# Optimization experiments

Measured on AMD Instinct MI355X. Metric: run time of the kernel, lower is better.

The kernel has to match this reference:

```python
import jax, jax.numpy as jnp
import numpy as np

B, N, D = 32, 181, 512          # batch, num_projs (seq len), embed_dim
H, HD = 8, 64                   # heads, head_dim
DEPTH, FFN = 6, 2048            # layers, mlp_ratio*embed_dim
MAXLEN = 181                    # RPE max_len (EncoderLayer default)
LN_EPS = 1e-5


def setup_inputs() -> dict:
    key = jax.random.key(0)
    ks = jax.random.split(key, 16)
    rn = lambda k, s, sc=0.02: (jax.random.normal(k, s, jnp.float32) * sc)
    return {
        "x_0": jax.random.normal(ks[0], (B, N, D), jnp.float32),
        "max_shift": 50,
        "pos_embed": rn(ks[1], (1, N, D)),
        "qkv_w": rn(ks[2], (DEPTH, D, 3 * D)), "qkv_b": jnp.zeros((DEPTH, 3 * D), jnp.float32),
        "out_w": rn(ks[3], (DEPTH, D, D)), "out_b": jnp.zeros((DEPTH, D), jnp.float32),
        "rel_pos": jax.random.normal(ks[4], (DEPTH, 2 * MAXLEN - 1, HD), jnp.float32),
        "rpe_w": rn(ks[5], (DEPTH, HD, 1)),
        "ln1_g": jnp.ones((DEPTH, D), jnp.float32), "ln1_b": jnp.zeros((DEPTH, D), jnp.float32),
        "ffn_w1": rn(ks[6], (DEPTH, D, FFN)), "ffn_b1": jnp.zeros((DEPTH, FFN), jnp.float32),
        "ffn_w2": rn(ks[7], (DEPTH, FFN, D)), "ffn_b2": jnp.zeros((DEPTH, D), jnp.float32),
        "ln2_g": jnp.ones((DEPTH, D), jnp.float32), "ln2_b": jnp.zeros((DEPTH, D), jnp.float32),
        "mlp_w1": rn(ks[8], (D, 64)), "mlp_b1": jnp.zeros((64,), jnp.float32),
        "mlp_w2": rn(ks[9], (64, 1)), "mlp_b2": jnp.zeros((1,), jnp.float32),
    }


def _layer_norm(x, g, b):
    m = jnp.mean(x, -1, keepdims=True)
    v = jnp.mean((x - m) ** 2, -1, keepdims=True)
    return (x - m) * jax.lax.rsqrt(v + LN_EPS) * g + b


def reference(x_0, max_shift, pos_embed, qkv_w, qkv_b, out_w, out_b, rel_pos, rpe_w,
              ln1_g, ln1_b, ffn_w1, ffn_b1, ffn_w2, ffn_b2, ln2_g, ln2_b,
              mlp_w1, mlp_b1, mlp_w2, mlp_b2):
    Bb, T, L = x_0.shape
    n_head = H
    hd = L // n_head
    scale = hd ** -0.5
    max_len = (rel_pos.shape[1] + 1) // 2
    # relative position index table [T, T]
    idx = jnp.arange(T)[None, :] - jnp.arange(T)[:, None] + (max_len - 1)

    x = x_0 + pos_embed
    depth = qkv_w.shape[0]
    for i in range(depth):
        # --- MHA with relative position bias ---
        qkv = (x @ qkv_w[i] + qkv_b[i]).reshape(Bb, T, 3, n_head, hd)
        q, k, v = qkv[:, :, 0], qkv[:, :, 1], qkv[:, :, 2]   # [B,T,H,hd]
        scores = jnp.einsum('bqhd,bkhd->bhqk', q, k) * scale
        bias = (rel_pos[i][idx] @ rpe_w[i])[..., 0]          # [T,T]
        scores = scores + bias[None, None]
        w = jax.nn.softmax(scores, axis=-1)
        attn = jnp.einsum('bhqk,bkhd->bqhd', w, v).reshape(Bb, T, L)
        attn = attn @ out_w[i] + out_b[i]
        x = _layer_norm(x + attn, ln1_g[i], ln1_b[i])
        # --- FFN ---
        h = jax.nn.gelu(x @ ffn_w1[i] + ffn_b1[i], approximate=False)
        h = h @ ffn_w2[i] + ffn_b2[i]
        x = _layer_norm(x + h, ln2_g[i], ln2_b[i])

    # per-projection shift head
    shift = jax.nn.relu(x @ mlp_w1 + mlp_b1) @ mlp_w2 + mlp_b2   # [B,T,1]

    # --- SpatialTransformer: bilinear warp along L only (flow[:,0] == 0) ---
    grid_y = 2.0 * (jnp.arange(T, dtype=jnp.float32) / (T - 1) - 0.5)   # [T]
    grid_x = 2.0 * (jnp.arange(L, dtype=jnp.float32) / (L - 1) - 0.5)   # [L]
    flow_x = shift * max_shift / (L // 2)                               # [B,T,1]
    gx = grid_x[None, None, :] + flow_x                                 # [B,T,L]
    # unnormalize (align_corners=False), border padding -> clamp coords
    ix = jnp.clip(((gx + 1.0) * L - 1.0) / 2.0, 0.0, L - 1.0)
    iy = jnp.clip(((grid_y + 1.0) * T - 1.0) / 2.0, 0.0, T - 1.0)       # [T]
    ix0f = jnp.floor(ix); wx = ix - ix0f
    iy0f = jnp.floor(iy); wy = iy - iy0f
    ix0 = jnp.clip(ix0f.astype(jnp.int32), 0, L - 1)
    ix1 = jnp.clip(ix0 + 1, 0, L - 1)
    iy0 = jnp.clip(iy0f.astype(jnp.int32), 0, T - 1)
    iy1 = jnp.clip(iy0 + 1, 0, T - 1)
    bidx = jnp.arange(Bb)[:, None, None]
    iy0b, iy1b = iy0[None, :, None], iy1[None, :, None]
    v00 = x_0[bidx, iy0b, ix0]; v01 = x_0[bidx, iy0b, ix1]
    v10 = x_0[bidx, iy1b, ix0]; v11 = x_0[bidx, iy1b, ix1]
    wyb = wy[None, :, None]
    warped = (1 - wyb) * ((1 - wx) * v00 + wx * v01) + wyb * ((1 - wx) * v10 + wx * v11)
    return shift, warped
```

## Files before the change

### kernel.cpp

```cpp
#include <hip/hip_runtime.h>
#include <hip/hip_bf16.h>
#include <math.h>

#define M_ROWS 5792
#define NTOK 181
#define NLAYER 6

typedef __attribute__((ext_vector_type(8))) _Float16 f16x8;
typedef __attribute__((ext_vector_type(4))) float f32x4;
typedef __attribute__((ext_vector_type(16))) float f32x16;

__device__ __forceinline__ ushort f2h(float f) {
    union { _Float16 h; ushort u; } v;
    v.h = (_Float16)f;
    return v.u;
}
__device__ __forceinline__ float h2f(ushort u) {
    union { ushort u; _Float16 h; } v; v.u = u;
    return (float)v.h;
}
__device__ __forceinline__ float gelu_f(float v) {
    return 0.5f * v * (1.0f + erff(v * 0.70710678118654752f));
}
__device__ __forceinline__ void async16(const void* g, void* l) {
    __builtin_amdgcn_global_load_lds((const __attribute__((address_space(1))) void*)g,
                                     (__attribute__((address_space(3))) void*)l, 16, 0, 0);
}

__global__ __launch_bounds__(256) void wt_kernel(const float* __restrict__ W,
                                                 ushort* __restrict__ Wt, int K, int N) {
    __shared__ float t[64][65];
    const size_t ls = (size_t)blockIdx.z * K * N;
    const float* Wl = W + ls;
    ushort* Wtl = Wt + ls;
    const int k0 = blockIdx.x * 64, n0 = blockIdx.y * 64;
    const int tr = threadIdx.x >> 6, tc = threadIdx.x & 63;
    #pragma unroll
    for (int i = 0; i < 16; ++i) {
        const int r = i * 4 + tr;
        t[r][tc] = Wl[(size_t)(k0 + r) * N + n0 + tc];
    }
    __syncthreads();
    #pragma unroll
    for (int i = 0; i < 16; ++i) {
        const int r = i * 4 + tr;
        Wtl[(size_t)(n0 + r) * K + k0 + tc] = f2h(t[tc][r]);
    }
}

__global__ void add_pos_kernel(const float* __restrict__ x0, const float* __restrict__ pos,
                               float* __restrict__ x, ushort* __restrict__ xb) {
    int idx = blockIdx.x * 256 + threadIdx.x;
    const int total = M_ROWS * 128;
    if (idx >= total) return;
    int col = idx & 127;
    int m   = idx >> 7;
    int t   = m % NTOK;
    float4 a = ((const float4*)x0)[idx];
    float4 p = ((const float4*)pos)[t * 128 + col];
    a.x += p.x; a.y += p.y; a.z += p.z; a.w += p.w;
    ((float4*)x)[idx] = a;
    ((ushort4*)xb)[idx] = make_ushort4(f2h(a.x), f2h(a.y), f2h(a.z), f2h(a.w));
}

template<int BM, int EPI, int SK>
__global__ __launch_bounds__(256) void mfma_gemm(const ushort* __restrict__ A,
                                                 const ushort* __restrict__ Bt,
                                                 const float* __restrict__ bias,
                                                 void* __restrict__ Cv,
                                                 int M, int K, int N) {
    constexpr int MREP = BM / 32;
    __shared__ __align__(16) ushort sA[2][BM * 32];
    __shared__ __align__(16) ushort sB[2][128 * 32];

    const int NC  = N >> 7;
    const int NR  = (M + BM - 1) / BM;
    const int NRP = (NR + 7) & ~7;
    const int PSB = NRP * NC;
    const int gid = blockIdx.x;
    const int sk  = (SK > 1) ? gid / PSB : 0;
    const int j   = (SK > 1) ? gid % PSB : gid;
    const int r   = (j / (8 * NC)) * 8 + (j & 7);
    const int c   = (j % (8 * NC)) >> 3;
    if (r >= NR) return;

    const int tid = threadIdx.x;
    const int lane = tid & 63;
    const int w = tid >> 6;
    const int wr = w >> 1, wc = w & 1;
    const int row0 = r * BM, col0 = c * 128;
    const int wbase = tid & ~63;

    f32x4 acc[MREP][4];
    const f32x4 zero = {0.f, 0.f, 0.f, 0.f};
    #pragma unroll
    for (int m = 0; m < MREP; ++m)
        #pragma unroll
        for (int n = 0; n < 4; ++n) acc[m][n] = zero;

    auto stage = [&](int buf, int kt) {
        const int k0 = kt << 5;
        #pragma unroll
        for (int i = 0; i < BM / 64; ++i) {
            const int s = i * 256 + tid;
            const int row = s >> 2;
            const int kbl = (s & 3) ^ ((row >> 1) & 3);
            int gr = row0 + row; if (gr > M - 1) gr = M - 1;
            async16(A + (size_t)gr * K + k0 + (kbl << 3),
                    &sA[buf][(i * 256 + wbase) * 8]);
        }
        #pragma unroll
        for (int i = 0; i < 2; ++i) {
            const int s = i * 256 + tid;
            const int nr = s >> 2;
            const int kbl = (s & 3) ^ ((nr >> 1) & 3);
            async16(Bt + (size_t)(col0 + nr) * K + k0 + (kbl << 3),
                    &sB[buf][(i * 256 + wbase) * 8]);
        }
    };

    const int NIT = (K / SK) >> 5;
    const int kt0 = sk * NIT;
    stage(0, kt0);
    const int l15 = lane & 15, kb = lane >> 4;
    for (int it = 0; it < NIT; ++it) {
        __syncthreads();
        if (it + 1 < NIT) stage((it + 1) & 1, kt0 + it + 1);
        const int buf = it & 1;
        f16x8 af[MREP], bfr[4];
        #pragma unroll
        for (int m = 0; m < MREP; ++m) {
            const int rr = wr * (BM / 2) + m * 16 + l15;
            af[m] = *(const f16x8*)&sA[buf][rr * 32 + ((kb ^ ((rr >> 1) & 3)) << 3)];
        }
        #pragma unroll
        for (int n = 0; n < 4; ++n) {
            const int rr = wc * 64 + n * 16 + l15;
            bfr[n] = *(const f16x8*)&sB[buf][rr * 32 + ((kb ^ ((rr >> 1) & 3)) << 3)];
        }
        #pragma unroll
        for (int m = 0; m < MREP; ++m)
            #pragma unroll
            for (int n = 0; n < 4; ++n)
                acc[m][n] = __builtin_amdgcn_mfma_f32_16x16x32_f16(af[m], bfr[n], acc[m][n], 0, 0, 0);
    }

    const int crow = row0 + wr * (BM / 2) + (lane >> 4) * 4;
    const int ccol = col0 + wc * 64 + l15;
    ushort* outh = (ushort*)Cv + (size_t)sk * M * N;
    #pragma unroll
    for (int m = 0; m < MREP; ++m)
        #pragma unroll
        for (int n = 0; n < 4; ++n) {
            const int gc = ccol + n * 16;
            const float bv = (SK == 1 || sk == 0) ? bias[gc] : 0.f;
            #pragma unroll
            for (int rr = 0; rr < 4; ++rr) {
                const int gr = crow + m * 16 + rr;
                if (gr < M) {
                    float v = acc[m][n][rr] + bv;
                    if (EPI == 1)      outh[(size_t)gr * N + gc] = f2h(gelu_f(v));
                    else if (EPI == 2) outh[(size_t)gr * N + gc] = f2h(v);
                    else               ((float*)Cv)[(size_t)gr * N + gc] = v;
                }
            }
        }
}

__global__ __launch_bounds__(256) void head_mfma(const ushort* __restrict__ A,
                                                 const ushort* __restrict__ Bt,
                                                 const float* __restrict__ b1,
                                                 const float* __restrict__ w2,
                                                 const float* __restrict__ b2,
                                                 float* __restrict__ shift) {
    const int M = M_ROWS, K = 512;
    __shared__ __align__(16) ushort sA[2][128 * 32];
    __shared__ __align__(16) ushort sB[2][64 * 32];
    const int tid = threadIdx.x;
    const int lane = tid & 63;
    const int w = tid >> 6;
    const int row0 = blockIdx.x * 128;
    const int wbase = tid & ~63;

    f32x4 acc[2][4];
    const f32x4 zero = {0.f, 0.f, 0.f, 0.f};
    #pragma unroll
    for (int m = 0; m < 2; ++m)
        #pragma unroll
        for (int n = 0; n < 4; ++n) acc[m][n] = zero;

    auto stage = [&](int buf, int kt) {
        const int k0 = kt << 5;
        #pragma unroll
        for (int i = 0; i < 2; ++i) {
            const int s = i * 256 + tid;
            const int row = s >> 2;
            const int kbl = (s & 3) ^ ((row >> 1) & 3);
            int gr = row0 + row; if (gr > M - 1) gr = M - 1;
            async16(A + (size_t)gr * K + k0 + (kbl << 3),
                    &sA[buf][(i * 256 + wbase) * 8]);
        }
        {
            const int s = tid;
            const int nr = s >> 2;
            const int kbl = (s & 3) ^ ((nr >> 1) & 3);
            async16(Bt + (size_t)nr * K + k0 + (kbl << 3),
                    &sB[buf][wbase * 8]);
        }
    };

    stage(0, 0);
    const int l15 = lane & 15, kb = lane >> 4;
    for (int it = 0; it < 16; ++it) {
        __syncthreads();
        if (it + 1 < 16) stage((it + 1) & 1, it + 1);
        const int buf = it & 1;
        f16x8 af[2], bfr[4];
        #pragma unroll
        for (int m = 0; m < 2; ++m) {
            const int r = w * 32 + m * 16 + l15;
            af[m] = *(const f16x8*)&sA[buf][r * 32 + ((kb ^ ((r >> 1) & 3)) << 3)];
        }
        #pragma unroll
        for (int n = 0; n < 4; ++n) {
            const int r = n * 16 + l15;
            bfr[n] = *(const f16x8*)&sB[buf][r * 32 + ((kb ^ ((r >> 1) & 3)) << 3)];
        }
        #pragma unroll
        for (int m = 0; m < 2; ++m)
            #pragma unroll
            for (int n = 0; n < 4; ++n)
                acc[m][n] = __builtin_amdgcn_mfma_f32_16x16x32_f16(af[m], bfr[n], acc[m][n], 0, 0, 0);
    }

    const float b2v = b2[0];
    float b1v[4], w2v[4];
    #pragma unroll
    for (int n = 0; n < 4; ++n) {
        const int c = n * 16 + l15;
        b1v[n] = b1[c];
        w2v[n] = w2[c];
    }
    #pragma unroll
    for (int m = 0; m < 2; ++m) {
        #pragma unroll
        for (int r = 0; r < 4; ++r) {
            float p = 0.f;
            #pragma unroll
            for (int n = 0; n < 4; ++n)
                p += fmaxf(acc[m][n][r] + b1v[n], 0.f) * w2v[n];
            #pragma unroll
            for (int off = 1; off < 16; off <<= 1) p += __shfl_xor(p, off);
            const int gr = row0 + w * 32 + m * 16 + kb * 4 + r;
            if (l15 == 0 && gr < M) shift[gr] = p + b2v;
        }
    }
}

__global__ void rbias_kernel(const float* __restrict__ rel_pos, const float* __restrict__ rpe_w,
                             float* __restrict__ r) {
    const int l = blockIdx.y;
    int j = blockIdx.x * 64 + threadIdx.x;
    if (j >= 2 * NTOK - 1) return;
    const float* rp = rel_pos + ((size_t)l * (2 * NTOK - 1) + j) * 64;
    const float* wv = rpe_w + l * 64;
    float s = 0.f;
    #pragma unroll
    for (int d = 0; d < 64; d += 4) {
        float4 a = *(const float4*)(rp + d);
        float4 b = *(const float4*)(wv + d);
        s += a.x*b.x + a.y*b.y + a.z*b.z + a.w*b.w;
    }
    r[l * 512 + j] = s;
}

__global__ __launch_bounds__(192, 2) void attn_mfma(const ushort* __restrict__ qkv,
                                                    const float* __restrict__ rb,
                                                    ushort* __restrict__ outb) {
    __shared__ __align__(16) ushort sm[18432];
    __shared__ __align__(16) ushort vt[12288];
    __shared__ float rs[416];
    const int b  = blockIdx.x >> 4;
    const int h  = (blockIdx.x >> 1) & 7;
    const int qh = blockIdx.x & 1;
    const int tid = threadIdx.x, lane = tid & 63, w = tid >> 6;
    const int l31 = lane & 31, hi = lane >> 5;
    const ushort* base = qkv + (size_t)(b * NTOK) * 1536 + h * 64;

    for (int i = tid; i < 416; i += 192) {
        int j = i - 32;
        rs[i] = (j >= 0 && j < 2 * NTOK - 1) ? rb[j] : 0.f;
    }
    #pragma unroll
    for (int i = 0; i < 8; ++i) {
        const int c = i * 192 + w * 64 + lane;
        const int k = c >> 3;
        int kg = k; if (kg > NTOK - 1) kg = NTOK - 1;
        const int dc = (c & 7) ^ (k & 7);
        async16(base + (size_t)kg * 1536 + 512 + dc * 8, &sm[(i * 192 + w * 64) * 8]);
    }
    #pragma unroll
    for (int i = 0; i < 4; ++i) {
        const int c = i * 192 + w * 64 + lane;
        const int ql = c >> 3;
        int qg = qh * 96 + ql; if (qg > NTOK - 1) qg = NTOK - 1;
        const int dc = (c & 7) ^ (ql & 7);
        async16(base + (size_t)qg * 1536 + dc * 8, &sm[12288 + (i * 192 + w * 64) * 8]);
    }
    #pragma unroll
    for (int i = 0; i < 8; ++i) {
        const int c = tid + i * 192;
        const int k = c >> 3, dcc = c & 7;
        const int kk = k < NTOK ? k : NTOK - 1;
        const uint4 v = *(const uint4*)(base + (size_t)kk * 1536 + 1024 + dcc * 8);
        const uint vv[4] = {v.x, v.y, v.z, v.w};
        #pragma unroll
        for (int j = 0; j < 4; ++j) {
            const int d0 = dcc * 8 + j * 2, d1 = d0 + 1;
            vt[d0 * 192 + ((((k >> 3) ^ ((d0 ^ (d0 >> 3)) & 7)) << 3) + (k & 7))] = (ushort)(vv[j] & 0xffffu);
            vt[d1 * 192 + ((((k >> 3) ^ ((d1 ^ (d1 >> 3)) & 7)) << 3) + (k & 7))] = (ushort)(vv[j] >> 16);
        }
    }
    __syncthreads();

    const int ql = 32 * w + l31;
    const int q  = qh * 96 + ql;
    f16x8 qf[4];
    #pragma unroll
    for (int ds = 0; ds < 4; ++ds)
        qf[ds] = *(const f16x8*)&sm[12288 + ql * 64 + (((2 * ds + hi) ^ (ql & 7)) << 3)];

    f32x16 S[6];
    #pragma unroll
    for (int kt = 0; kt < 6; ++kt)
        #pragma unroll
        for (int r = 0; r < 16; ++r) S[kt][r] = 0.f;
    #pragma unroll
    for (int kt = 0; kt < 6; ++kt) {
        const int krow = kt * 32 + l31;
        #pragma unroll
        for (int ds = 0; ds < 4; ++ds) {
            f16x8 kf = *(const f16x8*)&sm[krow * 64 + (((2 * ds + hi) ^ (krow & 7)) << 3)];
            S[kt] = __builtin_amdgcn_mfma_f32_32x32x16_f16(kf, qf[ds], S[kt], 0, 0, 0);
        }
    }

    float mx = -1e30f;
    #pragma unroll
    for (int kt = 0; kt < 6; ++kt)
        #pragma unroll
        for (int r = 0; r < 16; ++r) {
            const int k = kt * 32 + (r & 3) + 8 * (r >> 2) + 4 * hi;
            float s = (k < NTOK) ? S[kt][r] * 0.125f + rs[k - q + 212] : -1e30f;
            S[kt][r] = s;
            mx = fmaxf(mx, s);
        }
    mx = fmaxf(mx, __shfl_xor(mx, 32));
    float sum = 0.f;
    #pragma unroll
    for (int kt = 0; kt < 6; ++kt)
        #pragma unroll
        for (int r = 0; r < 16; ++r) {
            float e = __expf(S[kt][r] - mx);
            S[kt][r] = e;
            sum += e;
        }
    sum += __shfl_xor(sum, 32);
    const float inv = 1.0f / sum;

    __syncthreads();

    const int sq = (l31 ^ (l31 >> 3)) & 7;
    #pragma unroll
    for (int kt = 0; kt < 6; ++kt)
        #pragma unroll
        for (int r = 0; r < 16; r += 2) {
            const int k = kt * 32 + (r & 3) + 8 * (r >> 2) + 4 * hi;
            const uint pk = (uint)f2h(S[kt][r] * inv) | ((uint)f2h(S[kt][r + 1] * inv) << 16);
            *(uint*)&sm[w * 6144 + l31 * 192 + ((((k >> 3) ^ sq) << 3) + (k & 7))] = pk;
        }
    __syncthreads();

    f32x16 O[2];
    #pragma unroll
    for (int nt = 0; nt < 2; ++nt)
        #pragma unroll
        for (int r = 0; r < 16; ++r) O[nt][r] = 0.f;
    #pragma unroll
    for (int kt2 = 0; kt2 < 12; ++kt2) {
        f16x8 pa = *(const f16x8*)&sm[w * 6144 + l31 * 192 + ((((2 * kt2 + hi) ^ sq) << 3))];
        #pragma unroll
        for (int nt = 0; nt < 2; ++nt) {
            const int d = nt * 32 + l31;
            f16x8 vf = *(const f16x8*)&vt[d * 192 + (((2 * kt2 + hi) ^ ((d ^ (d >> 3)) & 7)) << 3)];
            O[nt] = __builtin_amdgcn_mfma_f32_32x32x16_f16(pa, vf, O[nt], 0, 0, 0);
        }
    }

    #pragma unroll
    for (int nt = 0; nt < 2; ++nt)
        #pragma unroll
        for (int r = 0; r < 16; ++r) {
            const int qr = qh * 96 + 32 * w + (r & 3) + 8 * (r >> 2) + 4 * hi;
            if (qr < NTOK)
                outb[(size_t)(b * NTOK + qr) * 512 + h * 64 + nt * 32 + l31] = f2h(O[nt][r]);
        }
}

template<int NY>
__global__ __launch_bounds__(256) void lnres_kernel(float* __restrict__ x, ushort* __restrict__ xb,
                                                    const ushort* __restrict__ y,
                                                    const ushort* __restrict__ y1,
                                                    const float* __restrict__ g, const float* __restrict__ bb) {
    const int row = blockIdx.x * 4 + (threadIdx.x >> 6);
    const int l = threadIdx.x & 63;
    float* xr = x + (size_t)row * 512;
    ushort* xbr = xb + (size_t)row * 512;
    const ushort* yr = y + (size_t)row * 512;
    float4 v0 = *(const float4*)(xr + (l << 2));
    float4 v1 = *(const float4*)(xr + 256 + (l << 2));
    const ushort4 u0 = *(const ushort4*)(yr + (l << 2));
    const ushort4 u1 = *(const ushort4*)(yr + 256 + (l << 2));
    v0.x += h2f(u0.x); v0.y += h2f(u0.y); v0.z += h2f(u0.z); v0.w += h2f(u0.w);
    v1.x += h2f(u1.x); v1.y += h2f(u1.y); v1.z += h2f(u1.z); v1.w += h2f(u1.w);
    if (NY == 2) {
        const ushort* y1r = y1 + (size_t)row * 512;
        const ushort4 w0 = *(const ushort4*)(y1r + (l << 2));
        const ushort4 w1 = *(const ushort4*)(y1r + 256 + (l << 2));
        v0.x += h2f(w0.x); v0.y += h2f(w0.y); v0.z += h2f(w0.z); v0.w += h2f(w0.w);
        v1.x += h2f(w1.x); v1.y += h2f(w1.y); v1.z += h2f(w1.z); v1.w += h2f(w1.w);
    }
    float s = v0.x + v0.y + v0.z + v0.w + v1.x + v1.y + v1.z + v1.w;
    #pragma unroll
    for (int off = 32; off; off >>= 1) s += __shfl_xor(s, off);
    const float m = s * (1.0f / 512.0f);
    float d0 = v0.x - m, d1 = v0.y - m, d2 = v0.z - m, d3 = v0.w - m;
    float d4 = v1.x - m, d5 = v1.y - m, d6 = v1.z - m, d7 = v1.w - m;
    float q = d0*d0 + d1*d1 + d2*d2 + d3*d3 + d4*d4 + d5*d5 + d6*d6 + d7*d7;
    #pragma unroll
    for (int off = 32; off; off >>= 1) q += __shfl_xor(q, off);
    const float r = rsqrtf(q * (1.0f / 512.0f) + 1e-5f);
    const float4 g0 = *(const float4*)(g + (l << 2));
    const float4 g1 = *(const float4*)(g + 256 + (l << 2));
    const float4 b0 = *(const float4*)(bb + (l << 2));
    const float4 b1 = *(const float4*)(bb + 256 + (l << 2));
    float4 o0, o1;
    o0.x = d0 * r * g0.x + b0.x; o0.y = d1 * r * g0.y + b0.y;
    o0.z = d2 * r * g0.z + b0.z; o0.w = d3 * r * g0.w + b0.w;
    o1.x = d4 * r * g1.x + b1.x; o1.y = d5 * r * g1.y + b1.y;
    o1.z = d6 * r * g1.z + b1.z; o1.w = d7 * r * g1.w + b1.w;
    *(float4*)(xr + (l << 2)) = o0;
    *(float4*)(xr + 256 + (l << 2)) = o1;
    *(ushort4*)(xbr + (l << 2)) = make_ushort4(f2h(o0.x), f2h(o0.y), f2h(o0.z), f2h(o0.w));
    *(ushort4*)(xbr + 256 + (l << 2)) = make_ushort4(f2h(o1.x), f2h(o1.y), f2h(o1.z), f2h(o1.w));
}

__global__ void warp_kernel(const float* __restrict__ x0, const float* __restrict__ shift,
                            const int* __restrict__ pms, float* __restrict__ warped) {
    int idx = blockIdx.x * 256 + threadIdx.x;
    if (idx >= M_ROWS * 512) return;
    int c = idx & 511;
    int m = idx >> 9;
    int t = m % NTOK;
    int b = m / NTOK;
    float max_shift = (float)pms[0];
    float sh = shift[m];
    float flow = sh * max_shift / 256.0f;
    float gx = 2.0f * ((float)c / 511.0f - 0.5f) + flow;
    float ix = ((gx + 1.0f) * 512.0f - 1.0f) * 0.5f;
    ix = fminf(fmaxf(ix, 0.0f), 511.0f);
    float gy = 2.0f * ((float)t / 180.0f - 0.5f);
    float iy = ((gy + 1.0f) * 181.0f - 1.0f) * 0.5f;
    iy = fminf(fmaxf(iy, 0.0f), 180.0f);
    float ix0f = floorf(ix), iy0f = floorf(iy);
    float wx = ix - ix0f, wy = iy - iy0f;
    int ix0 = min(max((int)ix0f, 0), 511);
    int ix1 = min(ix0 + 1, 511);
    int iy0 = min(max((int)iy0f, 0), 180);
    int iy1 = min(iy0 + 1, 180);
    const float* xb = x0 + (size_t)b * NTOK * 512;
    float v00 = xb[iy0 * 512 + ix0], v01 = xb[iy0 * 512 + ix1];
    float v10 = xb[iy1 * 512 + ix0], v11 = xb[iy1 * 512 + ix1];
    warped[idx] = (1.f - wy) * ((1.f - wx) * v00 + wx * v01) + wy * ((1.f - wx) * v10 + wx * v11);
}

extern "C" void kernel_launch(void* const* d_in, const int* in_sizes, int n_in,
                              void* d_out, int out_size, void* d_ws, size_t ws_size,
                              hipStream_t stream) {
    const float* x0   = (const float*)d_in[0];
    const int*   pms  = (const int*)d_in[1];
    const float* pos  = (const float*)d_in[2];
    const float* qkvw = (const float*)d_in[3];
    const float* qkvb = (const float*)d_in[4];
    const float* outw = (const float*)d_in[5];
    const float* outbp= (const float*)d_in[6];
    const float* relp = (const float*)d_in[7];
    const float* rpew = (const float*)d_in[8];
    const float* ln1g = (const float*)d_in[9];
    const float* ln1b = (const float*)d_in[10];
    const float* fw1  = (const float*)d_in[11];
    const float* fb1  = (const float*)d_in[12];
    const float* fw2  = (const float*)d_in[13];
    const float* fb2  = (const float*)d_in[14];
    const float* ln2g = (const float*)d_in[15];
    const float* ln2b = (const float*)d_in[16];
    const float* mw1  = (const float*)d_in[17];
    const float* mb1  = (const float*)d_in[18];
    const float* mw2  = (const float*)d_in[19];
    const float* mb2  = (const float*)d_in[20];

    float* out = (float*)d_out;

    char* ws = (char*)d_ws;
    float*  x     = (float*)ws;
    ushort* xb    = (ushort*)(ws + 11862016);
    char*   qr    = ws + 11862016 + 5931008;
    ushort* qkv   = (ushort*)qr;
    ushort* ybuf  = (ushort*)qr;
    ushort* ybuf2 = (ushort*)(qr + 5931008);
    ushort* hbuf  = (ushort*)(qr + 11862016);
    ushort* attnb = (ushort*)(qr + 35586048);
    float*  rbias = (float*)(qr + 35586048 + 5931008);
    ushort* wts   = (ushort*)(qr + 35586048 + 5931008 + 12288);
    ushort* qkv_wt = wts;
    ushort* out_wt = qkv_wt + 6 * 1536 * 512;
    ushort* f1_wt  = out_wt + 6 * 512 * 512;
    ushort* f2_wt  = f1_wt  + 6 * 512 * 2048;
    ushort* w1t    = f2_wt  + 6 * 2048 * 512;

    wt_kernel<<<dim3(8, 24, 6), 256, 0, stream>>>(qkvw, qkv_wt, 512, 1536);
    wt_kernel<<<dim3(8,  8, 6), 256, 0, stream>>>(outw, out_wt, 512, 512);
    wt_kernel<<<dim3(8, 32, 6), 256, 0, stream>>>(fw1,  f1_wt,  512, 2048);
    wt_kernel<<<dim3(32, 8, 6), 256, 0, stream>>>(fw2,  f2_wt,  2048, 512);
    wt_kernel<<<dim3(8,  1, 1), 256, 0, stream>>>(mw1,  w1t,    512, 64);
    rbias_kernel<<<dim3(6, 6), 64, 0, stream>>>(relp, rpew, rbias);

    add_pos_kernel<<<(M_ROWS * 128 + 255) / 256, 256, 0, stream>>>(x0, pos, x, xb);

    const int g_qkv  = 96 * 12;
    const int g_ffn1 = 96 * 16;
    const int g_np4  = 96 * 4;
    for (int i = 0; i < NLAYER; ++i) {
        mfma_gemm<64, 2, 1><<<g_qkv, 256, 0, stream>>>(xb, qkv_wt + (size_t)i * 1536 * 512,
                                                       qkvb + i * 1536, qkv, M_ROWS, 512, 1536);
        attn_mfma<<<512, 192, 0, stream>>>(qkv, rbias + i * 512, attnb);
        mfma_gemm<64, 2, 2><<<g_np4 * 2, 256, 0, stream>>>(attnb, out_wt + (size_t)i * 512 * 512,
                                                           outbp + i * 512, ybuf, M_ROWS, 512, 512);
        lnres_kernel<2><<<1448, 256, 0, stream>>>(x, xb, ybuf, ybuf2, ln1g + i * 512, ln1b + i * 512);
        mfma_gemm<64, 1, 1><<<g_ffn1, 256, 0, stream>>>(xb, f1_wt + (size_t)i * 2048 * 512,
                                                        fb1 + i * 2048, hbuf, M_ROWS, 512, 2048);
        mfma_gemm<64, 2, 2><<<g_np4 * 2, 256, 0, stream>>>(hbuf, f2_wt + (size_t)i * 512 * 2048,
                                                           fb2 + i * 512, ybuf, M_ROWS, 2048, 512);
        lnres_kernel<2><<<1448, 256, 0, stream>>>(x, xb, ybuf, ybuf2, ln2g + i * 512, ln2b + i * 512);
    }

    head_mfma<<<46, 256, 0, stream>>>(xb, w1t, mb1, mw2, mb2, out);
    warp_kernel<<<(M_ROWS * 512 + 255) / 256, 256, 0, stream>>>(x0, out, pms, out + M_ROWS);
}
```

Measured before the change: 786.8 us.

## Keep softmax probabilities in registers and vectorize V transpose into LDS

The attention kernel no longer writes P to LDS and reads it back. It builds the MFMA A-operand directly from the S accumulator registers with cross-half-wave shuffles, which removes two __syncthreads barriers. The V transpose now has each thread load 8 rows and write packed 16-byte chunks, replacing the scattered 2-byte LDS stores. s_setprio is also raised around the MFMA loops; the cost is more register pressure and extra shuffle instructions.

```diff
diff --git a/kernel.cpp b/kernel.cpp
--- a/kernel.cpp
+++ b/kernel.cpp
@@ -307,18 +307,29 @@
         const int dc = (c & 7) ^ (ql & 7);
         async16(base + (size_t)qg * 1536 + dc * 8, &sm[12288 + (i * 192 + w * 64) * 8]);
     }
-    #pragma unroll
-    for (int i = 0; i < 8; ++i) {
-        const int c = tid + i * 192;
-        const int k = c >> 3, dcc = c & 7;
-        const int kk = k < NTOK ? k : NTOK - 1;
-        const uint4 v = *(const uint4*)(base + (size_t)kk * 1536 + 1024 + dcc * 8);
-        const uint vv[4] = {v.x, v.y, v.z, v.w};
-        #pragma unroll
-        for (int j = 0; j < 4; ++j) {
-            const int d0 = dcc * 8 + j * 2, d1 = d0 + 1;
-            vt[d0 * 192 + ((((k >> 3) ^ ((d0 ^ (d0 >> 3)) & 7)) << 3) + (k & 7))] = (ushort)(vv[j] & 0xffffu);
-            vt[d1 * 192 + ((((k >> 3) ^ ((d1 ^ (d1 >> 3)) & 7)) << 3) + (k & 7))] = (ushort)(vv[j] >> 16);
+    {
+        const int k8 = tid % 24;
+        const int dc = tid / 24;
+        uint4 rowv[8];
+        #pragma unroll
+        for (int i = 0; i < 8; ++i) {
+            int kk = k8 * 8 + i; if (kk > NTOK - 1) kk = NTOK - 1;
+            rowv[i] = *(const uint4*)(base + (size_t)kk * 1536 + 1024 + dc * 8);
+        }
+        #pragma unroll
+        for (int j = 0; j < 8; ++j) {
+            const int d = dc * 8 + j;
+            const int sd = (d ^ (d >> 3)) & 7;
+            uint out[4];
+            #pragma unroll
+            for (int m = 0; m < 4; ++m) {
+                const uint lo  = ((const uint*)&rowv[2 * m    ])[j >> 1];
+                const uint hi2 = ((const uint*)&rowv[2 * m + 1])[j >> 1];
+                const uint a = (j & 1) ? (lo  >> 16) : (lo  & 0xffffu);
+                const uint bb = (j & 1) ? (hi2 >> 16) : (hi2 & 0xffffu);
+                out[m] = a | (bb << 16);
+            }
+            *(uint4*)&vt[d * 192 + ((k8 ^ sd) << 3)] = *(uint4*)out;
         }
     }
     __syncthreads();
@@ -335,6 +346,7 @@
     for (int kt = 0; kt < 6; ++kt)
         #pragma unroll
         for (int r = 0; r < 16; ++r) S[kt][r] = 0.f;
+    __builtin_amdgcn_s_setprio(1);
     #pragma unroll
     for (int kt = 0; kt < 6; ++kt) {
         const int krow = kt * 32 + l31;
@@ -344,6 +356,7 @@
             S[kt] = __builtin_amdgcn_mfma_f32_32x32x16_f16(kf, qf[ds], S[kt], 0, 0, 0);
         }
     }
+    __builtin_amdgcn_s_setprio(0);
 
     float mx = -1e30f;
     #pragma unroll
@@ -367,19 +380,10 @@
         }
     sum += __shfl_xor(sum, 32);
     const float inv = 1.0f / sum;
-
-    __syncthreads();
-
-    const int sq = (l31 ^ (l31 >> 3)) & 7;
     #pragma unroll
     for (int kt = 0; kt < 6; ++kt)
         #pragma unroll
-        for (int r = 0; r < 16; r += 2) {
-            const int k = kt * 32 + (r & 3) + 8 * (r >> 2) + 4 * hi;
-            const uint pk = (uint)f2h(S[kt][r] * inv) | ((uint)f2h(S[kt][r + 1] * inv) << 16);
-            *(uint*)&sm[w * 6144 + l31 * 192 + ((((k >> 3) ^ sq) << 3) + (k & 7))] = pk;
-        }
-    __syncthreads();
+        for (int r = 0; r < 16; ++r) S[kt][r] *= inv;
 
     f32x16 O[2];
     #pragma unroll
@@ -388,13 +392,28 @@
         for (int r = 0; r < 16; ++r) O[nt][r] = 0.f;
     #pragma unroll
     for (int kt2 = 0; kt2 < 12; ++kt2) {
-        f16x8 pa = *(const f16x8*)&sm[w * 6144 + l31 * 192 + ((((2 * kt2 + hi) ^ sq) << 3))];
+        const int kt = kt2 >> 1, half = kt2 & 1;
+        uint p[4];
+        #pragma unroll
+        for (int m = 0; m < 4; ++m)
+            p[m] = (uint)f2h(S[kt][8 * half + 2 * m]) |
+                   ((uint)f2h(S[kt][8 * half + 2 * m + 1]) << 16);
+        const uint s0l = (uint)__shfl_xor((int)p[0], 32);
+        const uint s0h = (uint)__shfl_xor((int)p[1], 32);
+        const uint s1l = (uint)__shfl_xor((int)p[2], 32);
+        const uint s1h = (uint)__shfl_xor((int)p[3], 32);
+        uint fa[4];
+        if (hi == 0) { fa[0] = p[0]; fa[1] = p[1]; fa[2] = s0l; fa[3] = s0h; }
+        else         { fa[0] = s1l; fa[1] = s1h; fa[2] = p[2]; fa[3] = p[3]; }
+        const f16x8 pa = *(const f16x8*)fa;
+        __builtin_amdgcn_s_setprio(1);
         #pragma unroll
         for (int nt = 0; nt < 2; ++nt) {
             const int d = nt * 32 + l31;
             f16x8 vf = *(const f16x8*)&vt[d * 192 + (((2 * kt2 + hi) ^ ((d ^ (d >> 3)) & 7)) << 3)];
             O[nt] = __builtin_amdgcn_mfma_f32_32x32x16_f16(pa, vf, O[nt], 0, 0, 0);
         }
+        __builtin_amdgcn_s_setprio(0);
     }
 
     #pragma unroll
```

Result: no change. 789.6 us (+0.4%).
